# Kernel tuning notes

Hardware: AMD Instinct MI355X
Metric: run time of the kernel (lower is better)

Reference implementation:

```python
import jax, jax.numpy as jnp
import numpy as np
import math

# ---- static configuration (mirrors FluidPCConfig defaults) ----
B, S, D = 8, 2048, 2048
N_LEVELS = 3
OUTER = 3            # fluid_outer_iters
HORIZON = 4          # mpc_horizon
INNER_STEPS = 5      # mpc_inner_steps
INNER_LR = 0.1       # mpc_inner_lr
CFL = 0.4            # cfl_target
KAPPA0 = 0.01        # kappa_init
LERAY_ITERS = 50     # leray_max_iter (fixed trip count; see notes)
REACT_STEPS = 1
REACT_ETA = 0.1
R2 = 1.4142135623730951


def _normalize(rho, eps=1e-8):
    rho = jnp.abs(rho) + eps
    return rho / jnp.sum(rho, axis=-1, keepdims=True)


def haar_dwt(x, n_levels):
    """Packed 1D Haar DWT along the sequence axis. x: (B,S,D) -> (B,S,D)."""
    a = x
    dets = []
    for _ in range(n_levels):
        e, o = a[:, 0::2], a[:, 1::2]
        dets.append((e - o) / R2)
        a = (e + o) / R2
    # layout: [approx_L, detail_L, detail_{L-1}, ..., detail_1]
    return jnp.concatenate([a] + dets[::-1], axis=1)


def haar_idwt(c, n_levels):
    """Inverse of haar_dwt. c: (B,S,D) -> (B,S,D)."""
    S_ = c.shape[1]
    a = c[:, : S_ >> n_levels]
    off = S_ >> n_levels
    for lev in range(n_levels, 0, -1):
        L = S_ >> lev
        d = c[:, off:off + L]
        off += L
        e, o = (a + d) / R2, (a - d) / R2
        a = jnp.stack([e, o], axis=2).reshape(c.shape[0], 2 * L, c.shape[2])
    return a


def coeffs_to_rho(c):
    # per-node scalar density from D-dim coefficients: (B,S,D) -> (B,S)
    return jnp.sqrt(jnp.sum(c * c, axis=-1))


# ---- periodic 1D graph operators on the S wavelet-coefficient nodes ----
def grad1(p):
    return jnp.roll(p, -1, axis=-1) - p


def div1(u):
    return u - jnp.roll(u, 1, axis=-1)


def lap1(p):
    return jnp.roll(p, -1, axis=-1) + jnp.roll(p, 1, axis=-1) - 2.0 * p


def leray(u):
    """Leray projection: u <- u - grad(p), lap(p)=div(u), Jacobi sweeps."""
    b = div1(u)
    def body(i, p):
        return 0.5 * (jnp.roll(p, -1, axis=-1) + jnp.roll(p, 1, axis=-1) - b)
    p = jax.lax.fori_loop(0, LERAY_ITERS, body, jnp.zeros_like(u))
    return u - grad1(p)


def rescale_dt(u):
    # per-batch dt so that achieved CFL == cfl_target: (B,S) -> (B,)
    return CFL / (jnp.max(jnp.abs(u), axis=-1) + 1e-8)


def advect(rho, u, dt, kappa):
    """Conservative upwind advection + kappa-weighted diffusion."""
    dt = dt[:, None]
    F = jnp.where(u > 0, u * rho, u * jnp.roll(rho, -1, axis=-1))
    return rho - dt * (F - jnp.roll(F, 1, axis=-1)) + kappa * dt * lap1(rho)


def mpc(rho, v):
    """Inner-gradient MPC drift (non-differentiable branch: stop_gradient)."""
    rho = jax.lax.stop_gradient(rho)
    v = jax.lax.stop_gradient(v)

    def cost(u):
        r = rho
        for _ in range(HORIZON):
            up = leray(u)
            r = _normalize(advect(r, up, rescale_dt(up), 0.0))
        # expected distance to value field
        return jnp.mean(jnp.sum((1.0 - v) * r, axis=-1))

    u = grad1(v)  # init drift toward high-value nodes
    g = jax.grad(cost)
    for _ in range(INNER_STEPS):
        u = u - INNER_LR * g(u)
    return u


def reaction(rho, phi):
    """Predictive-coding reaction: mirror-descent on potential+entropy."""
    for _ in range(REACT_STEPS):
        g = phi[None, :] + jnp.log(rho)
        rho = _normalize(rho * jnp.exp(-REACT_ETA * g))
    return rho


def kappa_at(k):
    # cosine anneal from KAPPA0 at k=0 to 0 at k=OUTER-1
    return 0.5 * KAPPA0 * (1.0 + math.cos(math.pi * k / (OUTER - 1)))


# static band index: node -> wavelet band (0=approx, 1..N_LEVELS=details)
_bi = np.zeros(S, dtype=np.int32)
_off = S >> N_LEVELS
for _i, _lev in enumerate(range(N_LEVELS, 0, -1)):
    _L = S >> _lev
    _bi[_off:_off + _L] = _i + 1
    _off += _L
BAND_IDX = jnp.asarray(_bi)


def setup_inputs() -> dict:
    key = jax.random.key(0)
    k1, k2, k3, k4 = jax.random.split(key, 4)
    return {
        "x": jax.random.normal(k1, (B, S, D), dtype=jnp.float32),
        "w_val": jax.random.normal(k2, (D,), dtype=jnp.float32) / np.float32(np.sqrt(D)),
        "phi": jax.random.normal(k3, (S,), dtype=jnp.float32) * 0.1,
        "band_w": jax.random.normal(k4, (N_LEVELS + 1, D), dtype=jnp.float32),
    }


def reference(x, w_val, phi, band_w):
    # density field from wavelet coefficients of x
    rho = _normalize(coeffs_to_rho(haar_dwt(x, N_LEVELS)))
    # value field: Linear(D,1) head, broadcast over D, DWT-packed, normalized
    per_token = jnp.einsum("bsd,d->bs", x, w_val)
    v_sig = jnp.broadcast_to(per_token[:, :, None], (B, S, D))
    v = _normalize(coeffs_to_rho(haar_dwt(v_sig, N_LEVELS)))

    for k in range(OUTER):
        rho = reaction(rho, phi)
        u = leray(mpc(rho, v))
        dt = rescale_dt(u)
        rho = _normalize(advect(rho, u, dt, kappa_at(k)))

    rho_f = rho + 0.1 * v
    rho_f = rho_f / jnp.sum(rho_f, axis=-1, keepdims=True)
    # readout: per-band learned D-vector, then inverse DWT -> (B,S,D)
    coeffs = rho_f[:, :, None] * band_w[BAND_IDX]
    return haar_idwt(coeffs, N_LEVELS)
```

## Files before the change

### kernel.cpp

```cpp
#include <hip/hip_runtime.h>
#include <math.h>

#define NSEQ 2048
#define EPSF 1e-8f
#define INV2R2 0.35355339059327373f
#define INVR2  0.7071067811865476f
#define NT 512

struct TapsAll { float lk65[65]; float lk2[97]; };

constexpr TapsAll make_taps() {
  TapsAll t{};
  double K[99] = {};
  for (int j = -49; j <= 49; ++j) {
    int aj = j < 0 ? -j : j;
    double term = 1.0;
    for (int q = 0; q < aj; ++q) term *= 0.5;
    double sum = term;
    for (int i = aj + 2; i <= 49; i += 2) {
      int m = (i + j) / 2;
      term *= (double)((i - 1) * i) / (4.0 * (double)m * (double)(i - m));
      sum += term;
    }
    K[j + 49] = -0.5 * sum;
  }
  double LKd[101] = {};
  for (int o = -50; o <= 50; ++o) {
    double km1 = (o - 1 >= -49 && o - 1 <= 49) ? K[o - 1 + 49] : 0.0;
    double k0  = (o     >= -49 && o     <= 49) ? K[o + 49]     : 0.0;
    double kp1 = (o + 1 >= -49 && o + 1 <= 49) ? K[o + 1 + 49] : 0.0;
    LKd[o + 50] = ((o == 0) ? 1.0 : 0.0) - (kp1 - 2.0 * k0 + km1);
  }
  for (int o = -32; o <= 32; ++o) t.lk65[o + 32] = (float)LKd[o + 50];
  for (int o = -48; o <= 48; ++o) {
    double s = 0.0;
    int alo = (o - 50 > -50) ? o - 50 : -50;
    int ahi = (o + 50 <  50) ? o + 50 :  50;
    for (int a = alo; a <= ahi; ++a) s += LKd[a + 50] * LKd[o - a + 50];
    t.lk2[o + 48] = (float)s;
  }
  return t;
}
constexpr TapsAll TAPS = make_taps();

__device__ __forceinline__ float rfl(float x) {
  return __int_as_float(__builtin_amdgcn_readfirstlane(__float_as_int(x)));
}

__device__ __forceinline__ float wave_sum(float x) {
#pragma unroll
  for (int m = 1; m < 64; m <<= 1) x += __shfl_xor(x, m, 64);
  return x;
}
__device__ __forceinline__ float wave_max(float x) {
#pragma unroll
  for (int m = 1; m < 64; m <<= 1) x = fmaxf(x, __shfl_xor(x, m, 64));
  return x;
}
__device__ __forceinline__ float block_sum(float x, float* red, int tid, int& gen) {
  float w = wave_sum(x);
  int slot = (gen & 7) << 5; gen++;
  if ((tid & 63) == 0) red[slot + (tid >> 6)] = w;
  __syncthreads();
  float4 a = *(float4*)(red + slot), b = *(float4*)(red + slot + 4);
  return rfl(((a.x + a.y) + (a.z + a.w)) + ((b.x + b.y) + (b.z + b.w)));
}
__device__ __forceinline__ void block_sum2(float a, float b, float* red, int tid, int& gen,
                                           float& oa, float& ob) {
  float wa = wave_sum(a), wb = wave_sum(b);
  int slot = (gen & 7) << 5; gen++;
  if ((tid & 63) == 0) { int w = tid >> 6; red[slot + w] = wa; red[slot + 16 + w] = wb; }
  __syncthreads();
  float4 a0 = *(float4*)(red + slot),      a1 = *(float4*)(red + slot + 4);
  float4 b0 = *(float4*)(red + slot + 16), b1 = *(float4*)(red + slot + 20);
  oa = rfl(((a0.x + a0.y) + (a0.z + a0.w)) + ((a1.x + a1.y) + (a1.z + a1.w)));
  ob = rfl(((b0.x + b0.y) + (b0.z + b0.w)) + ((b1.x + b1.y) + (b1.z + b1.w)));
}
__device__ __forceinline__ float sgnf(float x) {
  return (x > 0.f) ? 1.f : ((x < 0.f) ? -1.f : 0.f);
}

__device__ __forceinline__ void conv65(const float in[4], float acc[4],
                                       float* __restrict__ cb, int tid) {
  *(float4*)(cb + (tid << 2)) = make_float4(in[0], in[1], in[2], in[3]);
  __syncthreads();
  const int base = tid << 2;
  acc[0] = 0.f; acc[1] = 0.f; acc[2] = 0.f; acc[3] = 0.f;
#pragma unroll
  for (int m = 0; m < 17; ++m) {
    const int idx = (base - 32 + 4 * m) & (NSEQ - 1);
    const float4 c4 = *(const float4*)(cb + idx);
    const float cv[4] = {c4.x, c4.y, c4.z, c4.w};
#pragma unroll
    for (int jj = 0; jj < 4; ++jj) {
      const int d = 4 * m + jj;
#pragma unroll
      for (int j = 0; j < 4; ++j) {
        const int o = d - 32 - j;
        if (o >= -32 && o <= 32) acc[j] = fmaf(TAPS.lk65[o + 32], cv[jj], acc[j]);
      }
    }
  }
}

__device__ __forceinline__ void conv97(const float in[4], float acc[4],
                                       float* __restrict__ cb, int tid) {
  *(float4*)(cb + (tid << 2)) = make_float4(in[0], in[1], in[2], in[3]);
  __syncthreads();
  const int base = tid << 2;
  acc[0] = 0.f; acc[1] = 0.f; acc[2] = 0.f; acc[3] = 0.f;
#pragma unroll
  for (int m = 0; m < 25; ++m) {
    const int idx = (base - 48 + 4 * m) & (NSEQ - 1);
    const float4 c4 = *(const float4*)(cb + idx);
    const float cv[4] = {c4.x, c4.y, c4.z, c4.w};
#pragma unroll
    for (int jj = 0; jj < 4; ++jj) {
      const int d = 4 * m + jj;
#pragma unroll
      for (int j = 0; j < 4; ++j) {
        const int o = d - 48 - j;
        if (o >= -48 && o <= 48) acc[j] = fmaf(TAPS.lk2[o + 48], cv[jj], acc[j]);
      }
    }
  }
}

__global__ __launch_bounds__(256) void kA(const float* __restrict__ x,
                                          const float* __restrict__ wv,
                                          float* __restrict__ rho_us,
                                          float* __restrict__ pt) {
  const int blk = blockIdx.x;
  const int b = blk >> 8;
  const int g = blk & 255;
  const float* xb = x + (((size_t)b * NSEQ) + (size_t)g * 8) * 2048;
  const int tid = threadIdx.x;
  float sq[8] = {0.f, 0.f, 0.f, 0.f, 0.f, 0.f, 0.f, 0.f};
  float pp[8] = {0.f, 0.f, 0.f, 0.f, 0.f, 0.f, 0.f, 0.f};
  for (int c = tid * 4; c < 2048; c += 1024) {
    float4 w4 = *(const float4*)(wv + c);
    float wj[4] = {w4.x, w4.y, w4.z, w4.w};
    float xv[8][4];
#pragma unroll
    for (int r = 0; r < 8; ++r) {
      float4 t = *(const float4*)(xb + (size_t)r * 2048 + c);
      xv[r][0] = t.x; xv[r][1] = t.y; xv[r][2] = t.z; xv[r][3] = t.w;
    }
#pragma unroll
    for (int j = 0; j < 4; ++j) {
      float x0 = xv[0][j], x1 = xv[1][j], x2 = xv[2][j], x3 = xv[3][j];
      float x4 = xv[4][j], x5 = xv[5][j], x6 = xv[6][j], x7 = xv[7][j];
      float t01 = x0 + x1, t23 = x2 + x3, t45 = x4 + x5, t67 = x6 + x7;
      float a = t01 + t23, bb = t45 + t67;
      float c3 = a + bb, d3 = a - bb, d2a = t01 - t23, d2b = t45 - t67;
      float d10 = x0 - x1, d11 = x2 - x3, d12 = x4 - x5, d13 = x6 - x7;
      sq[0] += c3 * c3;  sq[1] += d3 * d3;  sq[2] += d2a * d2a; sq[3] += d2b * d2b;
      sq[4] += d10 * d10; sq[5] += d11 * d11; sq[6] += d12 * d12; sq[7] += d13 * d13;
      float w = wj[j];
      pp[0] += x0 * w; pp[1] += x1 * w; pp[2] += x2 * w; pp[3] += x3 * w;
      pp[4] += x4 * w; pp[5] += x5 * w; pp[6] += x6 * w; pp[7] += x7 * w;
    }
  }
  __shared__ float sred[4][16];
  float vals[16];
#pragma unroll
  for (int q = 0; q < 8; ++q) vals[q] = sq[q];
#pragma unroll
  for (int q = 0; q < 8; ++q) vals[8 + q] = pp[q];
#pragma unroll
  for (int q = 0; q < 16; ++q) vals[q] = wave_sum(vals[q]);
  int lane = tid & 63, wid = tid >> 6;
  if (lane == 0) {
#pragma unroll
    for (int q = 0; q < 16; ++q) sred[wid][q] = vals[q];
  }
  __syncthreads();
  if (tid < 16) {
    float s = sred[0][tid] + sred[1][tid] + sred[2][tid] + sred[3][tid];
    if (tid < 8) {
      float scale = (tid < 2) ? 0.125f : ((tid < 4) ? 0.25f : 0.5f);
      int pos = (tid == 0) ? g : (tid == 1) ? (256 + g)
               : (tid < 4) ? (512 + 2 * g + (tid - 2)) : (1024 + 4 * g + (tid - 4));
      rho_us[b * NSEQ + pos] = sqrtf(s * scale);
    } else {
      pt[b * NSEQ + 8 * g + (tid - 8)] = s;
    }
  }
}

__global__ __launch_bounds__(NT) void kB(const float* __restrict__ rho_us,
                                         const float* __restrict__ pt,
                                         const float* __restrict__ phi,
                                         float* __restrict__ rho_f) {
  __shared__ float cb[NSEQ];
  __shared__ float up0M[NSEQ];
  __shared__ float vE0[NT];
  __shared__ float rhoE0[NT], rhoE3[NT];
  __shared__ float upE3[NT];
  __shared__ float yE0[3][NT], yE3[3][NT];
  __shared__ float4 pairE[2][NT];
  __shared__ float red[256];
  __shared__ float red2[8];

  const int tid = threadIdx.x;
  const int b = blockIdx.x;
  const int tm1 = (tid - 1) & (NT - 1);
  const int tp1 = (tid + 1) & (NT - 1);
  int gen = 0;
  const float CFL_ = 0.4f;

  float4 phv = *(const float4*)(phi + 4 * tid);
  float ephi[4] = {__expf(-0.1f * phv.x), __expf(-0.1f * phv.y),
                   __expf(-0.1f * phv.z), __expf(-0.1f * phv.w)};

  float v_r[4];
  {
    const float* ptb = pt + b * NSEQ;
    float vl[4]; float part = 0.f;
#pragma unroll
    for (int j = 0; j < 4; ++j) {
      float c;
      if (tid < 64) {
        int r = (4 * tid + j) * 8;
        float t01 = ptb[r] + ptb[r+1], t23 = ptb[r+2] + ptb[r+3];
        float t45 = ptb[r+4] + ptb[r+5], t67 = ptb[r+6] + ptb[r+7];
        c = ((t01 + t23) + (t45 + t67)) * INV2R2;
      } else if (tid < 128) {
        int r = (4 * (tid - 64) + j) * 8;
        float t01 = ptb[r] + ptb[r+1], t23 = ptb[r+2] + ptb[r+3];
        float t45 = ptb[r+4] + ptb[r+5], t67 = ptb[r+6] + ptb[r+7];
        c = ((t01 + t23) - (t45 + t67)) * INV2R2;
      } else if (tid < 256) {
        int r = (4 * (tid - 128) + j) * 4;
        c = ((ptb[r] + ptb[r+1]) - (ptb[r+2] + ptb[r+3])) * 0.5f;
      } else {
        int r = (4 * (tid - 256) + j) * 2;
        c = (ptb[r] - ptb[r+1]) * INVR2;
      }
      float val = sqrtf(2048.0f * c * c) + EPSF;
      vl[j] = val; part += val;
    }
    float sv = block_sum(part, red, tid, gen);
    float inv = 1.0f / sv;
#pragma unroll
    for (int j = 0; j < 4; ++j) v_r[j] = vl[j] * inv;
    vE0[tid] = v_r[0];
  }
  float rho_r[4];
  {
    float4 rv = *(const float4*)(rho_us + b * NSEQ + 4 * tid);
    float rl[4] = {rv.x + EPSF, rv.y + EPSF, rv.z + EPSF, rv.w + EPSF};
    float part = rl[0] + rl[1] + rl[2] + rl[3];
    float sr = block_sum(part, red, tid, gen);
    float inv = 1.f / sr;
#pragma unroll
    for (int j = 0; j < 4; ++j) rho_r[j] = rl[j] * inv;
  }

  float up_r[4];
  float mx, mx0, um1c;
  {
    float vp4c = vE0[tp1];
    float u0[4] = {v_r[1] - v_r[0], v_r[2] - v_r[1], v_r[3] - v_r[2], vp4c - v_r[3]};
    conv65(u0, up_r, cb, tid);
    *(float4*)(up0M + (tid << 2)) = make_float4(up_r[0], up_r[1], up_r[2], up_r[3]);
    float mm = fmaxf(fmaxf(fabsf(up_r[0]), fabsf(up_r[1])),
                     fmaxf(fabsf(up_r[2]), fabsf(up_r[3])));
    mm = wave_max(mm);
    if ((tid & 63) == 0) red2[tid >> 6] = mm;
    __syncthreads();
    float4 r2a = *(float4*)(red2), r2b = *(float4*)(red2 + 4);
    mx = rfl(fmaxf(fmaxf(fmaxf(r2a.x, r2a.y), fmaxf(r2a.z, r2a.w)),
                   fmaxf(fmaxf(r2b.x, r2b.y), fmaxf(r2b.z, r2b.w))));
    um1c = up0M[(4 * tid - 1) & (NSEQ - 1)];
    mx0 = mx;
  }

  for (int k = 0; k < 3; ++k) {
    {
      float tl[4]; float part = 0.f;
#pragma unroll
      for (int j = 0; j < 4; ++j) {
        float r = rho_r[j];
        float t = r * ephi[j] * __expf(-0.1f * __logf(r));
        float t2 = fabsf(t) + EPSF;
        tl[j] = t2; part += t2;
      }
      float s = block_sum(part, red, tid, gen);
      float inv = 1.f / s;
#pragma unroll
      for (int j = 0; j < 4; ++j) rho_r[j] = tl[j] * inv;
      rhoE0[tid] = rho_r[0]; rhoE3[tid] = rho_r[3];
    }
    __syncthreads();
    const float rhom1 = rhoE3[tm1], rhop4 = rhoE0[tp1];
    if (k > 0) {
      float4 u4 = *(const float4*)(up0M + (tid << 2));
      up_r[0] = u4.x; up_r[1] = u4.y; up_r[2] = u4.z; up_r[3] = u4.w;
      um1c = up0M[(4 * tid - 1) & (NSEQ - 1)];
      mx = mx0;
    }

    float y_r[4][4];
    for (int step = 0; step < 5; ++step) {
      float dt = CFL_ / (mx + EPSF);
      float sarr[4]; float spv = 1.f; float ntie = 1.f, dot = 0.f;
#pragma unroll
      for (int h = 0; h < 4; ++h) {
        float invp = 1.f / spv;
        float rr[6];
        if (h == 0) {
          rr[0] = rhom1; rr[1] = rho_r[0]; rr[2] = rho_r[1];
          rr[3] = rho_r[2]; rr[4] = rho_r[3]; rr[5] = rhop4;
        } else {
          rr[0] = (fabsf(yE3[h-1][tm1]) + EPSF) * invp;
#pragma unroll
          for (int j = 0; j < 4; ++j) rr[j+1] = (fabsf(y_r[h-1][j]) + EPSF) * invp;
          rr[5] = (fabsf(yE0[h-1][tp1]) + EPSF) * invp;
        }
        float part2 = 0.f, aux = 0.f;
#pragma unroll
        for (int j = 0; j < 4; ++j) {
          float ri = rr[j+1], rim1 = rr[j], rip1 = rr[j+2];
          float ui = up_r[j], um = j ? up_r[j-1] : um1c;
          float Fi = ui > 0.f ? ui * ri : ui * rip1;
          float Fm = um > 0.f ? um * rim1 : um * ri;
          float yv = ri - dt * (Fi - Fm);
          y_r[h][j] = yv;
          float ayv = fabsf(yv) + EPSF;
          part2 += ayv;
          if (h == 0) aux += (fabsf(ui) == mx) ? 1.f : 0.f;
          if (h == 3) aux += (1.f - v_r[j]) * 0.125f * ayv;
        }
        if (h < 3) { yE0[h][tid] = y_r[h][0]; yE3[h][tid] = y_r[h][3]; }
        if (h == 3) {
          float sg0 = sgnf(y_r[3][0]), sg3 = sgnf(y_r[3][3]);
          pairE[1][tid] = make_float4(sg0 * (1.f - v_r[0]) * 0.125f, sg0,
                                      sg3 * (1.f - v_r[3]) * 0.125f, sg3);
        }
        if (h == 0) { float o1, o2; block_sum2(part2, aux, red, tid, gen, o1, o2); sarr[0] = o1; ntie = o2; }
        else if (h == 3) { float o1, o2; block_sum2(part2, aux, red, tid, gen, o1, o2); sarr[3] = o1; dot = o2 / o1; }
        else sarr[h] = block_sum(part2, red, tid, gen);
        spv = sarr[h];
      }
      float wreg[4], upbar[4];
#pragma unroll
      for (int j = 0; j < 4; ++j) { wreg[j] = (1.f - v_r[j]) * 0.125f; upbar[j] = 0.f; }
      float dtb_part = 0.f;
#pragma unroll
      for (int h = 3; h >= 0; --h) {
        float invst = 1.f / sarr[h];
        float invp = (h > 0) ? 1.f / sarr[h-1] : 0.f;
        const int bo = h & 1;
        float yb_r[4];
#pragma unroll
        for (int j = 0; j < 4; ++j)
          yb_r[j] = sgnf(y_r[h][j]) * (wreg[j] - dot) * invst;
        float4 pm = pairE[bo][tm1], pp = pairE[bo][tp1];
        float ybm1 = (pm.z - dot * pm.w) * invst;
        float ybp4 = (pp.x - dot * pp.y) * invst;
        float rr[6];
        if (h == 0) {
          rr[0] = rhom1; rr[1] = rho_r[0]; rr[2] = rho_r[1];
          rr[3] = rho_r[2]; rr[4] = rho_r[3]; rr[5] = rhop4;
        } else {
          rr[0] = (fabsf(yE3[h-1][tm1]) + EPSF) * invp;
#pragma unroll
          for (int j = 0; j < 4; ++j) rr[j+1] = (fabsf(y_r[h-1][j]) + EPSF) * invp;
          rr[5] = (fabsf(yE0[h-1][tp1]) + EPSF) * invp;
        }
        float dotn = 0.f;
#pragma unroll
        for (int j = 0; j < 4; ++j) {
          float ri = rr[j+1], rim1 = rr[j], rip1 = rr[j+2];
          float ui = up_r[j], um = j ? up_r[j-1] : um1c;
          float ybi = yb_r[j];
          float ybm = j ? yb_r[j-1] : ybm1;
          float ybp = (j < 3) ? yb_r[j+1] : ybp4;
          float Fbi = dt * (ybp - ybi);
          float Fbm = dt * (ybi - ybm);
          float wn = ybi;
          if (ui > 0.f)    wn += Fbi * ui;
          if (!(um > 0.f)) wn += Fbm * um;
          upbar[j] += Fbi * (ui > 0.f ? ri : rip1);
          float Fi = ui > 0.f ? ui * ri : ui * rip1;
          float Fm = um > 0.f ? um * rim1 : um * ri;
          dtb_part -= ybi * (Fi - Fm);
          if (h > 0) dotn += wn * ri;
          wreg[j] = wn;
        }
        if (h > 0) {
          float sgA = sgnf(y_r[h-1][0]), sgB = sgnf(y_r[h-1][3]);
          pairE[(h - 1) & 1][tid] = make_float4(sgA * wreg[0], sgA, sgB * wreg[3], sgB);
          dot = block_sum(dotn, red, tid, gen);
        }
      }
      float dtbar = block_sum(dtb_part, red, tid, gen);
      float md = mx + EPSF;
      float mbar = dtbar * (-CFL_ / (md * md));
      float tiesc = mbar / ntie;
#pragma unroll
      for (int j = 0; j < 4; ++j) {
        float ui = up_r[j];
        if (fabsf(ui) == mx) upbar[j] += tiesc * sgnf(ui);
      }
      float accv[4];
      conv97(upbar, accv, cb, tid);
#pragma unroll
      for (int j = 0; j < 4; ++j) up_r[j] -= 0.1f * accv[j];
      upE3[tid] = up_r[3];
      {
        float mm = fmaxf(fmaxf(fabsf(up_r[0]), fabsf(up_r[1])),
                         fmaxf(fabsf(up_r[2]), fabsf(up_r[3])));
        mm = wave_max(mm);
        if ((tid & 63) == 0) red2[tid >> 6] = mm;
      }
      __syncthreads();
      float4 r2a = *(float4*)(red2), r2b = *(float4*)(red2 + 4);
      mx = rfl(fmaxf(fmaxf(fmaxf(r2a.x, r2a.y), fmaxf(r2a.z, r2a.w)),
                     fmaxf(fmaxf(r2b.x, r2b.y), fmaxf(r2b.z, r2b.w))));
      um1c = upE3[tm1];
    }
    float dt = CFL_ / (mx + EPSF);
    float kap = (k == 0) ? 0.01f : ((k == 1) ? 0.005f : 0.0f);
    float rr[6];
    rr[0] = rhom1; rr[1] = rho_r[0]; rr[2] = rho_r[1];
    rr[3] = rho_r[2]; rr[4] = rho_r[3]; rr[5] = rhop4;
    float ylc[4]; float p2 = 0.f;
#pragma unroll
    for (int j = 0; j < 4; ++j) {
      float ri = rr[j+1], rim1 = rr[j], rip1 = rr[j+2];
      float ui = up_r[j], um = j ? up_r[j-1] : um1c;
      float Fi = ui > 0.f ? ui * ri : ui * rip1;
      float Fm = um > 0.f ? um * rim1 : um * ri;
      float yv = ri - dt * (Fi - Fm) + kap * dt * (rip1 + rim1 - 2.f * ri);
      ylc[j] = yv; p2 += fabsf(yv) + EPSF;
    }
    float s = block_sum(p2, red, tid, gen);
    float inv = 1.f / s;
#pragma unroll
    for (int j = 0; j < 4; ++j) rho_r[j] = (fabsf(ylc[j]) + EPSF) * inv;
  }
  {
    float fl[4]; float part = 0.f;
#pragma unroll
    for (int j = 0; j < 4; ++j) {
      float f = rho_r[j] + 0.1f * v_r[j];
      fl[j] = f; part += f;
    }
    float s = block_sum(part, red, tid, gen);
    float inv = 1.f / s;
    *(float4*)(rho_f + b * NSEQ + 4 * tid) =
        make_float4(fl[0] * inv, fl[1] * inv, fl[2] * inv, fl[3] * inv);
  }
}

__global__ __launch_bounds__(256) void kC(const float* __restrict__ rho_f,
                                          const float* __restrict__ bw,
                                          float* __restrict__ out) {
  const int blk = blockIdx.x;
  const int b = blk >> 8;
  const int g = blk & 255;
  __shared__ float q[8];
  if (threadIdx.x < 8) {
    int t = threadIdx.x;
    const float* rb = rho_f + b * NSEQ;
    float val;
    if (t == 0)      val = rb[g] * INV2R2;
    else if (t == 1) val = rb[256 + g] * INV2R2;
    else if (t < 4)  val = rb[512 + 2 * g + (t - 2)] * 0.5f;
    else             val = rb[1024 + 4 * g + (t - 4)] * INVR2;
    q[t] = val;
  }
  __syncthreads();
  float* ob = out + (((size_t)b * NSEQ) + (size_t)g * 8) * 2048;
  for (int c = threadIdx.x * 4; c < 2048; c += 1024) {
    float4 B0 = *(const float4*)(bw + c);
    float4 B1 = *(const float4*)(bw + 2048 + c);
    float4 B2 = *(const float4*)(bw + 4096 + c);
    float4 B3 = *(const float4*)(bw + 6144 + c);
    float b0[4] = {B0.x, B0.y, B0.z, B0.w};
    float b1[4] = {B1.x, B1.y, B1.z, B1.w};
    float b2[4] = {B2.x, B2.y, B2.z, B2.w};
    float b3[4] = {B3.x, B3.y, B3.z, B3.w};
    float o[8][4];
#pragma unroll
    for (int cc = 0; cc < 4; ++cc) {
      float pa = q[0] * b0[cc], pd3 = q[1] * b1[cc];
      float p2a = q[2] * b2[cc], p2b = q[3] * b2[cc];
      float e0 = pa + pd3, e1 = pa - pd3;
      float f0 = e0 + p2a, f1 = e0 - p2a, f2 = e1 + p2b, f3 = e1 - p2b;
      float g0 = q[4] * b3[cc], g1 = q[5] * b3[cc], g2 = q[6] * b3[cc], g3 = q[7] * b3[cc];
      o[0][cc] = f0 + g0; o[1][cc] = f0 - g0;
      o[2][cc] = f1 + g1; o[3][cc] = f1 - g1;
      o[4][cc] = f2 + g2; o[5][cc] = f2 - g2;
      o[6][cc] = f3 + g3; o[7][cc] = f3 - g3;
    }
#pragma unroll
    for (int j = 0; j < 8; ++j) {
      float4 t = make_float4(o[j][0], o[j][1], o[j][2], o[j][3]);
      *(float4*)(ob + (size_t)j * 2048 + c) = t;
    }
  }
}

extern "C" void kernel_launch(void* const* d_in, const int* in_sizes, int n_in,
                              void* d_out, int out_size, void* d_ws, size_t ws_size,
                              hipStream_t stream) {
  (void)in_sizes; (void)n_in; (void)out_size; (void)ws_size;
  const float* x   = (const float*)d_in[0];
  const float* wv  = (const float*)d_in[1];
  const float* phi = (const float*)d_in[2];
  const float* bw  = (const float*)d_in[3];
  float* out = (float*)d_out;
  float* rho_us = (float*)d_ws;
  float* pt     = rho_us + 8 * NSEQ;
  float* rho_f  = pt + 8 * NSEQ;

  kA<<<dim3(2048), dim3(256), 0, stream>>>(x, wv, rho_us, pt);
  kB<<<dim3(8), dim3(NT), 0, stream>>>(rho_us, pt, phi, rho_f);
  kC<<<dim3(2048), dim3(256), 0, stream>>>(rho_f, bw, out);
}
```

Measured before the change: 166.4 us.

## Truncate gradient conv taps, merge dtbar reduction with conv barrier, apply ties sparsely

Shrinks the precomputed squared-operator convolution from 97 to 81 taps, cutting LDS reads and FMAs per MPC step. The dtbar block reduction is folded into the same barrier as the upbar write, and the tie correction is applied after the convolution by scattering each tied index's contribution through a shared list built with atomics. The post-normalisation barrier is also removed by reading neighbour halos before normalisation and scaling them. Risks include accuracy loss from the shorter tap window and correctness concerns around the atomic tie buffer and the counter reset.

```diff
diff --git a/kernel.cpp b/kernel.cpp
--- a/kernel.cpp
+++ b/kernel.cpp
@@ -7,7 +7,7 @@
 #define INVR2  0.7071067811865476f
 #define NT 512
 
-struct TapsAll { float lk65[65]; float lk2[97]; };
+struct TapsAll { float lk65[65]; float lk2[81]; };
 
 constexpr TapsAll make_taps() {
   TapsAll t{};
@@ -32,12 +32,12 @@
     LKd[o + 50] = ((o == 0) ? 1.0 : 0.0) - (kp1 - 2.0 * k0 + km1);
   }
   for (int o = -32; o <= 32; ++o) t.lk65[o + 32] = (float)LKd[o + 50];
-  for (int o = -48; o <= 48; ++o) {
+  for (int o = -40; o <= 40; ++o) {
     double s = 0.0;
     int alo = (o - 50 > -50) ? o - 50 : -50;
     int ahi = (o + 50 <  50) ? o + 50 :  50;
     for (int a = alo; a <= ahi; ++a) s += LKd[a + 50] * LKd[o - a + 50];
-    t.lk2[o + 48] = (float)s;
+    t.lk2[o + 40] = (float)s;
   }
   return t;
 }
@@ -103,15 +103,13 @@
   }
 }
 
-__device__ __forceinline__ void conv97(const float in[4], float acc[4],
-                                       float* __restrict__ cb, int tid) {
-  *(float4*)(cb + (tid << 2)) = make_float4(in[0], in[1], in[2], in[3]);
-  __syncthreads();
+__device__ __forceinline__ void conv81_read(float acc[4], const float* __restrict__ cb,
+                                            int tid) {
   const int base = tid << 2;
   acc[0] = 0.f; acc[1] = 0.f; acc[2] = 0.f; acc[3] = 0.f;
 #pragma unroll
-  for (int m = 0; m < 25; ++m) {
-    const int idx = (base - 48 + 4 * m) & (NSEQ - 1);
+  for (int m = 0; m < 21; ++m) {
+    const int idx = (base - 40 + 4 * m) & (NSEQ - 1);
     const float4 c4 = *(const float4*)(cb + idx);
     const float cv[4] = {c4.x, c4.y, c4.z, c4.w};
 #pragma unroll
@@ -119,8 +117,8 @@
       const int d = 4 * m + jj;
 #pragma unroll
       for (int j = 0; j < 4; ++j) {
-        const int o = d - 48 - j;
-        if (o >= -48 && o <= 48) acc[j] = fmaf(TAPS.lk2[o + 48], cv[jj], acc[j]);
+        const int o = d - 40 - j;
+        if (o >= -40 && o <= 40) acc[j] = fmaf(TAPS.lk2[o + 40], cv[jj], acc[j]);
       }
     }
   }
@@ -200,7 +198,9 @@
   __shared__ float yE0[3][NT], yE3[3][NT];
   __shared__ float4 pairE[2][NT];
   __shared__ float red[256];
-  __shared__ float red2[8];
+  __shared__ float red2[16];
+  __shared__ int   tieBufI[NSEQ];
+  __shared__ int   tieCnt;
 
   const int tid = threadIdx.x;
   const int b = blockIdx.x;
@@ -208,6 +208,8 @@
   const int tp1 = (tid + 1) & (NT - 1);
   int gen = 0;
   const float CFL_ = 0.4f;
+
+  if (tid == 0) tieCnt = 0;
 
   float4 phv = *(const float4*)(phi + 4 * tid);
   float ephi[4] = {__expf(-0.1f * phv.x), __expf(-0.1f * phv.y),
@@ -277,6 +279,7 @@
   }
 
   for (int k = 0; k < 3; ++k) {
+    float rhom1, rhop4;
     {
       float tl[4]; float part = 0.f;
 #pragma unroll
@@ -286,14 +289,14 @@
         float t2 = fabsf(t) + EPSF;
         tl[j] = t2; part += t2;
       }
+      rhoE0[tid] = tl[0]; rhoE3[tid] = tl[3];
       float s = block_sum(part, red, tid, gen);
       float inv = 1.f / s;
 #pragma unroll
       for (int j = 0; j < 4; ++j) rho_r[j] = tl[j] * inv;
-      rhoE0[tid] = rho_r[0]; rhoE3[tid] = rho_r[3];
-    }
-    __syncthreads();
-    const float rhom1 = rhoE3[tm1], rhop4 = rhoE0[tp1];
+      rhom1 = rhoE3[tm1] * inv;
+      rhop4 = rhoE0[tp1] * inv;
+    }
     if (k > 0) {
       float4 u4 = *(const float4*)(up0M + (tid << 2));
       up_r[0] = u4.x; up_r[1] = u4.y; up_r[2] = u4.z; up_r[3] = u4.w;
@@ -395,17 +398,39 @@
           dot = block_sum(dotn, red, tid, gen);
         }
       }
-      float dtbar = block_sum(dtb_part, red, tid, gen);
-      float md = mx + EPSF;
-      float mbar = dtbar * (-CFL_ / (md * md));
-      float tiesc = mbar / ntie;
+      *(float4*)(cb + (tid << 2)) = make_float4(upbar[0], upbar[1], upbar[2], upbar[3]);
+      {
+        float w = wave_sum(dtb_part);
+        if ((tid & 63) == 0) red2[8 + (tid >> 6)] = w;
+      }
 #pragma unroll
       for (int j = 0; j < 4; ++j) {
         float ui = up_r[j];
-        if (fabsf(ui) == mx) upbar[j] += tiesc * sgnf(ui);
-      }
+        if (fabsf(ui) == mx) {
+          int ix = atomicAdd(&tieCnt, 1);
+          tieBufI[ix] = (4 * tid + j) | ((ui < 0.f) ? 0x10000 : 0);
+        }
+      }
+      __syncthreads();
+      float4 r2c = *(float4*)(red2 + 8), r2d = *(float4*)(red2 + 12);
+      float dtbar = rfl(((r2c.x + r2c.y) + (r2c.z + r2c.w)) +
+                        ((r2d.x + r2d.y) + (r2d.z + r2d.w)));
+      float md = mx + EPSF;
+      float tiesc = (dtbar * (-CFL_ / (md * md))) / ntie;
       float accv[4];
-      conv97(upbar, accv, cb, tid);
+      conv81_read(accv, cb, tid);
+      int nt = (int)(ntie + 0.5f);
+      for (int e = 0; e < nt; ++e) {
+        int ent = tieBufI[e];
+        int p = ent & 0xFFFF;
+        float sg = (ent & 0x10000) ? -tiesc : tiesc;
+#pragma unroll
+        for (int j = 0; j < 4; ++j) {
+          int d = ((4 * tid + j) - p) & (NSEQ - 1);
+          int ds = (d >= 1024) ? d - 2048 : d;
+          if (ds >= -40 && ds <= 40) accv[j] = fmaf(sg, TAPS.lk2[ds + 40], accv[j]);
+        }
+      }
 #pragma unroll
       for (int j = 0; j < 4; ++j) up_r[j] -= 0.1f * accv[j];
       upE3[tid] = up_r[3];
@@ -415,6 +440,7 @@
         mm = wave_max(mm);
         if ((tid & 63) == 0) red2[tid >> 6] = mm;
       }
+      if (tid == 0) tieCnt = 0;
       __syncthreads();
       float4 r2a = *(float4*)(red2), r2b = *(float4*)(red2 + 4);
       mx = rfl(fmaxf(fmaxf(fmaxf(r2a.x, r2a.y), fmaxf(r2a.z, r2a.w)),
```

Result: no change. 165.5 us (-0.5%).
